# Performance work log

Hardware: AMD Instinct MI355X
Metric: run time of the kernel (lower is better)

## Reference

```python
import jax, jax.numpy as jnp
import numpy as np
from jax import lax

H = 64  # hidden_size == embedding_size


def gru_last_hidden(emb, W_ih, W_hh, b_ih, b_hh):
    """PyTorch single-layer GRU over seq [L, H]; returns final hidden [H].
    Gate order in stacked weights: r, z, n (PyTorch convention)."""
    def step(h, x):
        gi = W_ih @ x + b_ih            # [3H]
        gh = W_hh @ h + b_hh            # [3H]
        i_r, i_z, i_n = jnp.split(gi, 3)
        h_r, h_z, h_n = jnp.split(gh, 3)
        r = jax.nn.sigmoid(i_r + h_r)
        z = jax.nn.sigmoid(i_z + h_z)
        n = jnp.tanh(i_n + r * h_n)
        h_new = (1.0 - z) * n + z * h
        return h_new, None
    h0 = jnp.zeros((H,), dtype=emb.dtype)
    h_last, _ = lax.scan(step, h0, emb)
    return h_last


def setup_inputs() -> dict:
    key = jax.random.key(0)
    ks = jax.random.split(key, 12)
    N, D, A, V, L = 256, 128, 40, 128, 16
    F3_IN = N * (D + H + N)
    s = 0.02
    return {
        "obs": jax.random.normal(ks[0], (N, D), dtype=jnp.float32),
        "token_ids": jax.random.randint(ks[1], (L,), 0, V),
        "emb_table": jax.random.normal(ks[2], (V, H), dtype=jnp.float32) * s,
        "gru_Wih": jax.random.normal(ks[3], (3 * H, H), dtype=jnp.float32) * s,
        "gru_Whh": jax.random.normal(ks[4], (3 * H, H), dtype=jnp.float32) * s,
        "gru_bih": jnp.zeros((3 * H,), dtype=jnp.float32),
        "gru_bhh": jnp.zeros((3 * H,), dtype=jnp.float32),
        "f1_W": jax.random.normal(ks[5], (H, 2 * D), dtype=jnp.float32) * s,
        "f1_b": jnp.zeros((H,), dtype=jnp.float32),
        "f3_W1": jax.random.normal(ks[6], (512, F3_IN), dtype=jnp.float32) * s,
        "f3_b1": jnp.zeros((512,), dtype=jnp.float32),
        "f3_W2": jax.random.normal(ks[7], (A, 512), dtype=jnp.float32) * s,
        "f3_b2": jnp.zeros((A,), dtype=jnp.float32),
    }


def reference(obs, token_ids, emb_table, gru_Wih, gru_Whh, gru_bih, gru_bhh,
              f1_W, f1_b, f3_W1, f3_b1, f3_W2, f3_b2):
    N = obs.shape[0]
    # Encoder: embedding lookup + GRU, keep last timestep output
    emb = emb_table[token_ids]                       # [L, H]
    g_tilde = gru_last_hidden(emb, gru_Wih, gru_Whh, gru_bih, gru_bhh)  # [H]

    # Pairwise f1 + dot with g_tilde. f1(concat(o_i,o_j)) @ g = obs_i@Wa.T@g
    # + obs_j@Wb.T@g + b@g  (exact factorization of the linear over pairs).
    Wa, Wb = jnp.split(f1_W, 2, axis=1)              # each [H, D]
    u = obs @ (Wa.T @ g_tilde)                       # [N]  (outer index a)
    v = obs @ (Wb.T @ g_tilde)                       # [N]  (inner index b)
    Z = u[:, None] + v[None, :] + jnp.dot(f1_b, g_tilde)   # [N, N]

    # softmax over ALL N^2 entries (torch Softmax(dim=0) on the flat stack)
    p = jax.nn.softmax(Z.reshape(-1)).reshape(N, N)

    g_rep = jnp.broadcast_to(g_tilde, (N, H))
    x = jnp.concatenate([obs, g_rep, p], axis=1).reshape(-1)  # [N*(D+H+N)]

    h1 = jax.nn.relu(f3_W1 @ x + f3_b1)
    return f3_W2 @ h1 + f3_b2                         # [action_shape]
```

## Files before the change

kernel.cpp:

```cpp
#include <hip/hip_runtime.h>
#include <math.h>

#define H    64
#define N    256
#define D    128
#define L    16
#define SEG4   112
#define F3IN (N * 448)
#define CG4   1792

typedef float v4f __attribute__((ext_vector_type(4)));

__device__ __forceinline__ float sigmoidf_(float x) {
    return 1.0f / (1.0f + expf(-x));
}
__device__ __forceinline__ float dot4(float4 a, float4 b) {
    return a.x * b.x + a.y * b.y + a.z * b.z + a.w * b.w;
}
__device__ __forceinline__ float dotv(v4f a, v4f b) {
    return a[0] * b[0] + a[1] * b[1] + a[2] * b[2] + a[3] * b[3];
}

__global__ __launch_bounds__(256, 1) void k_enc(
    const int* __restrict__ token_ids, const float* __restrict__ emb_table,
    const float* __restrict__ Wih, const float* __restrict__ Whh,
    const float* __restrict__ bih, const float* __restrict__ bhh,
    const float* __restrict__ f1W, const float* __restrict__ obs,
    float* __restrict__ g_out, float* __restrict__ eus_out,
    float* __restrict__ ev_out)
{
    __shared__ float emb_s[L * H];
    __shared__ float gi_all[L * 192];
    __shared__ float h_s[H];
    __shared__ float gh_s[192];
    __shared__ float wa_s[D];
    __shared__ float wb_s[D];
    __shared__ float red[256];
    __shared__ float red2[256];

    const int k = threadIdx.x;

    {
        int tok = token_ids[k >> 4];
        ((float4*)emb_s)[k] = ((const float4*)emb_table)[tok * 16 + (k & 15)];
    }
    if (k < H) h_s[k] = 0.0f;

    float4 wih4[16], whh4[16];
    float bi = 0.0f, bh = 0.0f;
    if (k < 192) {
        const float4* wi = (const float4*)(Wih + k * H);
        const float4* wh = (const float4*)(Whh + k * H);
#pragma unroll
        for (int c = 0; c < 16; ++c) { wih4[c] = wi[c]; whh4[c] = wh[c]; }
        bi = bih[k]; bh = bhh[k];
    }

    float f1wreg[64];
#pragma unroll
    for (int kk = 0; kk < 64; ++kk) f1wreg[kk] = f1W[kk * 256 + k];

    __syncthreads();

    if (k < 192) {
        float gi[L];
#pragma unroll
        for (int tt = 0; tt < L; ++tt) gi[tt] = bi;
#pragma unroll
        for (int c = 0; c < 16; ++c) {
            float4 w = wih4[c];
#pragma unroll
            for (int tt = 0; tt < L; ++tt)
                gi[tt] += dot4(w, ((const float4*)(emb_s + tt * 64))[c]);
        }
#pragma unroll
        for (int tt = 0; tt < L; ++tt) gi_all[tt * 192 + k] = gi[tt];
    }
    __syncthreads();

    for (int tt = 0; tt < L; ++tt) {
        if (k < 192) {
            const float4* hv = (const float4*)h_s;
            float a0 = 0, a1 = 0, a2 = 0, a3 = 0;
#pragma unroll
            for (int c = 0; c < 16; c += 4) {
                a0 += dot4(whh4[c],     hv[c]);
                a1 += dot4(whh4[c + 1], hv[c + 1]);
                a2 += dot4(whh4[c + 2], hv[c + 2]);
                a3 += dot4(whh4[c + 3], hv[c + 3]);
            }
            gh_s[k] = (a0 + a1) + (a2 + a3) + bh;
        }
        __syncthreads();
        if (k < H) {
            float r = sigmoidf_(gi_all[tt * 192 + k] + gh_s[k]);
            float z = sigmoidf_(gi_all[tt * 192 + 64 + k] + gh_s[64 + k]);
            float n = tanhf(gi_all[tt * 192 + 128 + k] + r * gh_s[128 + k]);
            h_s[k] = (1.0f - z) * n + z * h_s[k];
        }
        __syncthreads();
    }

    {
        float s = 0.0f;
#pragma unroll
        for (int kk = 0; kk < 64; ++kk) s += f1wreg[kk] * h_s[kk];
        if (k < D) wa_s[k] = s;
        else       wb_s[k - D] = s;
        if (k < H) g_out[k] = h_s[k];
    }
    __syncthreads();

    float4 orow[32];
    {
        const float4* rp = (const float4*)(obs + k * D);
#pragma unroll
        for (int c = 0; c < 32; ++c) orow[c] = rp[c];
    }
    float u = 0.0f, v = 0.0f;
#pragma unroll
    for (int c = 0; c < 32; ++c) {
        u += dot4(orow[c], ((const float4*)wa_s)[c]);
        v += dot4(orow[c], ((const float4*)wb_s)[c]);
    }

    red[k] = u; red2[k] = v; __syncthreads();
    for (int s = 128; s > 0; s >>= 1) {
        if (k < s) { red[k] = fmaxf(red[k], red[k + s]); red2[k] = fmaxf(red2[k], red2[k + s]); }
        __syncthreads();
    }
    const float mu = red[0], mv = red2[0];
    __syncthreads();
    const float eui = expf(u - mu), evi = expf(v - mv);
    red[k] = eui; red2[k] = evi; __syncthreads();
    for (int s = 128; s > 0; s >>= 1) {
        if (k < s) { red[k] += red[k + s]; red2[k] += red2[k + s]; }
        __syncthreads();
    }
    const float Su = red[0], Sv = red2[0];

    eus_out[k] = eui * (1.0f / (Su * Sv));
    ev_out[k]  = evi;
}

__global__ __launch_bounds__(256, 4) void k_mv(
    const float* __restrict__ W1, const float* __restrict__ obs,
    const float* __restrict__ g, const float* __restrict__ eus,
    const float* __restrict__ ev, float* __restrict__ partial)
{
    const int t  = threadIdx.x;
    const int cg = blockIdx.x & 15;
    const int rg = blockIdx.x >> 4;

    v4f xr[7];
    {
        const float4* obs4 = (const float4*)obs;
        const float4* g4   = (const float4*)g;
        const float4* ev4  = (const float4*)ev;
#pragma unroll
        for (int j = 0; j < 7; ++j) {
            int idx = t + j * 256;
            int s   = idx / SEG4;
            int c   = idx - s * SEG4;
            int seg = cg * 16 + s;
            float4 o;
            if (c < 32)       o = obs4[seg * 32 + c];
            else if (c < 48)  o = g4[c - 32];
            else {
                float4 e = ev4[c - 48];
                float m = eus[seg];
                o = make_float4(e.x * m, e.y * m, e.z * m, e.w * m);
            }
            xr[j] = (v4f){o.x, o.y, o.z, o.w};
        }
    }

    const v4f* w0 = (const v4f*)W1 + (size_t)(rg * 2) * (F3IN / 4)
                  + (size_t)cg * CG4 + t;
    const v4f* w1 = w0 + (F3IN / 4);

    float s0a = 0.0f, s0b = 0.0f, s1a = 0.0f, s1b = 0.0f;
#pragma unroll
    for (int j = 0; j < 7; ++j) {
        v4f wa = __builtin_nontemporal_load(w0 + j * 256);
        v4f wb = __builtin_nontemporal_load(w1 + j * 256);
        float da = dotv(wa, xr[j]);
        float db = dotv(wb, xr[j]);
        if (j & 1) { s0b += da; s1b += db; }
        else       { s0a += da; s1a += db; }
    }
    float sums[2] = { s0a + s0b, s1a + s1b };

    __shared__ float red[2][4];
    const int wave = t >> 6, lane = t & 63;
#pragma unroll
    for (int rr = 0; rr < 2; ++rr) {
        float s = sums[rr];
#pragma unroll
        for (int off = 32; off > 0; off >>= 1) s += __shfl_down(s, off, 64);
        if (lane == 0) red[rr][wave] = s;
    }
    __syncthreads();
    if (t < 2)
        partial[(rg * 2 + t) * 16 + cg] =
            red[t][0] + red[t][1] + red[t][2] + red[t][3];
}

__global__ __launch_bounds__(512) void k_finish(
    const float* __restrict__ partial, const float* __restrict__ b1,
    const float* __restrict__ W2, const float* __restrict__ b2,
    float* __restrict__ out)
{
    __shared__ float h1s[512];
    const int r = threadIdx.x;
    {
        const float4* p4 = (const float4*)(partial + r * 16);
        float4 A = p4[0], B = p4[1], C = p4[2], E = p4[3];
        float s = (A.x + A.y + A.z + A.w) + (B.x + B.y + B.z + B.w)
                + (C.x + C.y + C.z + C.w) + (E.x + E.y + E.z + E.w);
        h1s[r] = fmaxf(s + b1[r], 0.0f);
    }
    __syncthreads();

    const int wave = r >> 6, lane = r & 63;
    for (int row = wave; row < 40; row += 8) {
        float s = 0.0f;
#pragma unroll
        for (int c = 0; c < 8; ++c)
            s += W2[row * 512 + lane + c * 64] * h1s[lane + c * 64];
#pragma unroll
        for (int off = 32; off > 0; off >>= 1) s += __shfl_down(s, off, 64);
        if (lane == 0) out[row] = s + b2[row];
    }
}

extern "C" void kernel_launch(void* const* d_in, const int* in_sizes, int n_in,
                              void* d_out, int out_size, void* d_ws, size_t ws_size,
                              hipStream_t stream)
{
    const float* obs       = (const float*)d_in[0];
    const int*   token_ids = (const int*)  d_in[1];
    const float* emb_table = (const float*)d_in[2];
    const float* Wih       = (const float*)d_in[3];
    const float* Whh       = (const float*)d_in[4];
    const float* bih       = (const float*)d_in[5];
    const float* bhh       = (const float*)d_in[6];
    const float* f1W       = (const float*)d_in[7];
    const float* W1        = (const float*)d_in[9];
    const float* b1        = (const float*)d_in[10];
    const float* W2        = (const float*)d_in[11];
    const float* b2        = (const float*)d_in[12];

    float* ws      = (float*)d_ws;
    float* g       = ws;
    float* eus     = ws + 64;
    float* ev      = ws + 320;
    float* partial = ws + 640;
    float* out     = (float*)d_out;

    k_enc<<<1, 256, 0, stream>>>(token_ids, emb_table, Wih, Whh, bih, bhh,
                                 f1W, obs, g, eus, ev);
    k_mv<<<4096, 256, 0, stream>>>(W1, obs, g, eus, ev, partial);
    k_finish<<<1, 512, 0, stream>>>(partial, b1, W2, b2, out);
}
```

Before: 71.94 us.

## Use wave shuffles for encoder softmax reductions and per-wave contiguous W1 chunks

The encoder's shared-memory tree reductions for max and sum become wave-level xor shuffles plus a small cross-wave combine, which removes many block barriers from the single-block serial kernel. In the matvec kernel each wave now reads its own contiguous 448-float4 chunk of W1 instead of block-strided rows. The nontemporal load hints are replaced by plain loads. The access-pattern and cache-hint changes affect how the large W1 stream hits DRAM and the caches, and could help or hurt.

```diff
diff --git a/kernel.cpp b/kernel.cpp
--- a/kernel.cpp
+++ b/kernel.cpp
@@ -35,10 +35,10 @@
     __shared__ float gh_s[192];
     __shared__ float wa_s[D];
     __shared__ float wb_s[D];
-    __shared__ float red[256];
-    __shared__ float red2[256];
+    __shared__ float wred[4][4];
 
     const int k = threadIdx.x;
+    const int wave = k >> 6, lane = k & 63;
 
     {
         int tok = token_ids[k >> 4];
@@ -124,20 +124,28 @@
         v += dot4(orow[c], ((const float4*)wb_s)[c]);
     }
 
-    red[k] = u; red2[k] = v; __syncthreads();
-    for (int s = 128; s > 0; s >>= 1) {
-        if (k < s) { red[k] = fmaxf(red[k], red[k + s]); red2[k] = fmaxf(red2[k], red2[k + s]); }
-        __syncthreads();
-    }
-    const float mu = red[0], mv = red2[0];
-    __syncthreads();
+    float um = u, vm = v;
+#pragma unroll
+    for (int off = 32; off > 0; off >>= 1) {
+        um = fmaxf(um, __shfl_xor(um, off, 64));
+        vm = fmaxf(vm, __shfl_xor(vm, off, 64));
+    }
+    if (lane == 0) { wred[0][wave] = um; wred[1][wave] = vm; }
+    __syncthreads();
+    const float mu = fmaxf(fmaxf(wred[0][0], wred[0][1]), fmaxf(wred[0][2], wred[0][3]));
+    const float mv = fmaxf(fmaxf(wred[1][0], wred[1][1]), fmaxf(wred[1][2], wred[1][3]));
+
     const float eui = expf(u - mu), evi = expf(v - mv);
-    red[k] = eui; red2[k] = evi; __syncthreads();
-    for (int s = 128; s > 0; s >>= 1) {
-        if (k < s) { red[k] += red[k + s]; red2[k] += red2[k + s]; }
-        __syncthreads();
-    }
-    const float Su = red[0], Sv = red2[0];
+    float us = eui, vs = evi;
+#pragma unroll
+    for (int off = 32; off > 0; off >>= 1) {
+        us += __shfl_xor(us, off, 64);
+        vs += __shfl_xor(vs, off, 64);
+    }
+    if (lane == 0) { wred[2][wave] = us; wred[3][wave] = vs; }
+    __syncthreads();
+    const float Su = (wred[2][0] + wred[2][1]) + (wred[2][2] + wred[2][3]);
+    const float Sv = (wred[3][0] + wred[3][1]) + (wred[3][2] + wred[3][3]);
 
     eus_out[k] = eui * (1.0f / (Su * Sv));
     ev_out[k]  = evi;
@@ -151,6 +159,7 @@
     const int t  = threadIdx.x;
     const int cg = blockIdx.x & 15;
     const int rg = blockIdx.x >> 4;
+    const int wave = t >> 6, lane = t & 63;
 
     v4f xr[7];
     {
@@ -159,7 +168,7 @@
         const float4* ev4  = (const float4*)ev;
 #pragma unroll
         for (int j = 0; j < 7; ++j) {
-            int idx = t + j * 256;
+            int idx = wave * 448 + j * 64 + lane;
             int s   = idx / SEG4;
             int c   = idx - s * SEG4;
             int seg = cg * 16 + s;
@@ -176,14 +185,14 @@
     }
 
     const v4f* w0 = (const v4f*)W1 + (size_t)(rg * 2) * (F3IN / 4)
-                  + (size_t)cg * CG4 + t;
+                  + (size_t)cg * CG4 + wave * 448 + lane;
     const v4f* w1 = w0 + (F3IN / 4);
 
     float s0a = 0.0f, s0b = 0.0f, s1a = 0.0f, s1b = 0.0f;
 #pragma unroll
     for (int j = 0; j < 7; ++j) {
-        v4f wa = __builtin_nontemporal_load(w0 + j * 256);
-        v4f wb = __builtin_nontemporal_load(w1 + j * 256);
+        v4f wa = w0[j * 64];
+        v4f wb = w1[j * 64];
         float da = dotv(wa, xr[j]);
         float db = dotv(wb, xr[j]);
         if (j & 1) { s0b += da; s1b += db; }
@@ -192,7 +201,6 @@
     float sums[2] = { s0a + s0b, s1a + s1b };
 
     __shared__ float red[2][4];
-    const int wave = t >> 6, lane = t & 63;
 #pragma unroll
     for (int rr = 0; rr < 2; ++rr) {
         float s = sums[rr];
```

New measurement: 73.58 us. +2.3%, slower.
